# Kernel tuning notes

Hardware: AMD Instinct MI355X
Metric: run time of the kernel (lower is better)

The kernel has to match this reference:

```python
import jax, jax.numpy as jnp
import numpy as np

B, N, D, H, K = 16, 256, 64, 64, 2  # batch, nodes, d_in, d_hidden, top_k


def setup_inputs() -> dict:
    key = jax.random.key(0)
    k0, k1, k2 = jax.random.split(key, 3)
    O = jax.random.normal(k0, (B, N, D), dtype=jnp.float32)
    # PairwiseFeaturizer.proj: Linear(4*D, H) -> ReLU -> Linear(H, 1)
    W1 = jax.random.normal(k1, (4 * D, H), dtype=jnp.float32) / np.sqrt(4 * D).astype(np.float32)
    b1 = jnp.zeros((H,), dtype=jnp.float32)
    W2 = jax.random.normal(k2, (H, 1), dtype=jnp.float32) / np.sqrt(H).astype(np.float32)
    b2 = jnp.zeros((1,), dtype=jnp.float32)
    return {"O": O, "W1": W1, "b1": b1, "W2": W2, "b2": b2}


def reference(O, W1, b1, W2, b2):
    Bn, Nn, d = O.shape
    ii, jj = jnp.triu_indices(Nn, k=1)  # all undirected pairs i<j, M = N(N-1)/2
    Oi = O[:, ii, :]  # (B, M, d) gather
    Oj = O[:, jj, :]  # (B, M, d) gather
    feats = jnp.concatenate([Oi, Oj, jnp.abs(Oi - Oj), Oi * Oj], axis=-1)  # (B, M, 4d)
    h = jax.nn.relu(jnp.einsum('bmf,fh->bmh', feats, W1) + b1)
    Q = (jnp.einsum('bmh,ho->bmo', h, W2) + b2)[..., 0]  # (B, M)
    # greedy top-k selection mask (eps -> 0 limit of select_pairs)
    idx = jax.lax.top_k(Q, K)[1]  # (B, K)
    mask = jnp.zeros(Q.shape, dtype=bool).at[jnp.arange(Q.shape[0])[:, None], idx].set(True)
    return Q, mask
```

## Files before the change

kernel.cpp:

```cpp
#include <hip/hip_runtime.h>
#include <math.h>

#define Bn 16
#define Nn 256
#define Mm (Nn*(Nn-1)/2)
#define CHUNK 4080

typedef __attribute__((ext_vector_type(8))) _Float16 f16x8;
typedef __attribute__((ext_vector_type(4))) _Float16 f16x4;
typedef __attribute__((ext_vector_type(4))) float f32x4;
typedef __attribute__((ext_vector_type(16))) float f32x16;

typedef union { f16x8 v; _Float16 h[8]; unsigned u[4]; } H8;
typedef union { f16x4 v; _Float16 h[4]; } H4;

#define MFMA(acc, a, b) \
  acc = __builtin_amdgcn_mfma_f32_16x16x32_f16((a), (b), (acc), 0, 0, 0)
#define MFMA32(acc, a, b) \
  acc = __builtin_amdgcn_mfma_f32_32x32x16_f16((a), (b), (acc), 0, 0, 0)

__device__ __forceinline__ void top2_update(float v, int m,
    float& v1, int& i1, float& v2, int& i2)
{
  bool c1 = (v > v1) || (v == v1 && m < i1);
  bool c2 = (v > v2) || (v == v2 && m < i2);
  float nv2 = c1 ? v1 : (c2 ? v : v2);
  int   ni2 = c1 ? i1 : (c2 ? m : i2);
  v1 = c1 ? v : v1;  i1 = c1 ? m : i1;
  v2 = nv2;          i2 = ni2;
}

__device__ __forceinline__ int hperm(int h) {
  return (h >> 5) * 32 + ((h >> 2) & 1) * 16 + (h & 3) + 4 * ((h & 31) >> 3);
}

__global__ __launch_bounds__(256) void prep_all(
    const float* __restrict__ O, const float* __restrict__ W1,
    const float* __restrict__ b1,
    _Float16* __restrict__ wtg, _Float16* __restrict__ obg,
    float* __restrict__ Ag, _Float16* __restrict__ Cgh)
{
  const int t = threadIdx.x;
  if (blockIdx.x < 64) {
    const int h = blockIdx.x;
    wtg[h * 256 + t] = (_Float16)W1[t * 64 + h];
    return;
  }

  __shared__ __align__(16) _Float16 s_ob[64][72];
  __shared__ __align__(16) _Float16 s_w[64][136];
  const int l = t & 63, wv = t >> 6;
  const int lo = l & 15, g = l >> 4;
  const int bb = blockIdx.x - 64;
  const int b = bb >> 2, rt = bb & 3;
  const int r0 = rt * 64;
  const float* Ob = O + ((size_t)b * Nn + r0) * 64;

  #pragma unroll
  for (int p = 0; p < 4; ++p) {
    int v = t + p * 256;
    int r = v >> 4, c4 = (v & 15) * 4;
    float4 x = ((const float4*)Ob)[v];
    H4 pk; pk.h[0] = (_Float16)x.x; pk.h[1] = (_Float16)x.y;
           pk.h[2] = (_Float16)x.z; pk.h[3] = (_Float16)x.w;
    *(f16x4*)&s_ob[r][c4] = pk.v;
    *(f16x4*)&obg[((size_t)b * Nn + r0 + r) * 64 + c4] = pk.v;
  }
  #pragma unroll
  for (int p = 0; p < 32; ++p) {
    int kk = p * 4 + (t >> 6), h = t & 63;
    s_w[h][kk] = (_Float16)W1[kk * 64 + h];
  }
  __syncthreads();

  H8 aop[2];
  #pragma unroll
  for (int ks = 0; ks < 2; ++ks)
    aop[ks].v = *(const f16x8*)&s_ob[wv * 16 + lo][ks * 32 + g * 8];

  #pragma unroll
  for (int half = 0; half < 2; ++half) {
    #pragma unroll
    for (int nf = 0; nf < 4; ++nf) {
      f32x4 ac = {0.f, 0.f, 0.f, 0.f};
      #pragma unroll
      for (int ks = 0; ks < 2; ++ks) {
        H8 bop; bop.v = *(const f16x8*)&s_w[nf * 16 + lo][half * 64 + ks * 32 + g * 8];
        MFMA(ac, aop[ks].v, bop.v);
      }
      const int h  = nf * 16 + lo;
      const int px = hperm(h);
      if (half == 0) {
        float bbv = b1[h];
        #pragma unroll
        for (int r = 0; r < 4; ++r)
          Ag[((size_t)b * Nn + r0 + wv * 16 + g * 4 + r) * 64 + px] = ac[r] + bbv;
      } else {
        #pragma unroll
        for (int r = 0; r < 4; ++r)
          Cgh[((size_t)b * Nn + r0 + wv * 16 + g * 4 + r) * 64 + px] = (_Float16)ac[r];
      }
    }
  }
}

__global__ __launch_bounds__(256, 2) void pair_kernel(
    const _Float16* __restrict__ obg,
    const float* __restrict__ Ag,
    const _Float16* __restrict__ Cgh,
    const float* __restrict__ W2,
    const float* __restrict__ b2,
    const _Float16* __restrict__ wtg,
    float* __restrict__ Q,
    float* __restrict__ cand)
{
  __shared__ __align__(16) _Float16 s_wt[64][136];
  __shared__ __align__(16) _Float16 s_oi[16][72];
  __shared__ __align__(16) float s_Ap[16][68];
  __shared__ float s_w2p[64];
  __shared__ float s_red[4][4];

  const int t  = threadIdx.x;
  const int l  = t & 63, wv = t >> 6;
  const int lo32 = l & 31, hi = l >> 5;

  const int blk    = blockIdx.x;
  const int within = blk >> 3;
  const int batch  = (blk & 7) * 2 + within / 72;
  int tl           = within % 72;
  int a = 0;
  while (tl >= 8 - (a >> 1)) { tl -= 8 - (a >> 1); ++a; }
  const int c   = (a >> 1) + tl;
  const int ti0 = a * 16, tj0 = c * 32;
  const bool isdiag = (tj0 < ti0 + 16);

  const size_t obase = (size_t)batch * Nn;
  const size_t qbase = (size_t)batch * Mm;

  {
    const int h = t >> 2, kq = (t & 3) * 32;
    #pragma unroll
    for (int q = 0; q < 4; ++q)
      *(f16x8*)&s_wt[h][kq + q * 8] =
          *(const f16x8*)&wtg[h * 256 + 128 + kq + q * 8];
  }
  {
    int r = t >> 4, c4 = (t & 15) * 4;
    *(f16x4*)&s_oi[r][c4] =
        *(const f16x4*)&obg[(obase + ti0 + r) * 64 + c4];
    *(f32x4*)&s_Ap[r][c4] =
        *(const f32x4*)&Ag[(obase + ti0 + r) * 64 + c4];
    if (t < 64) s_w2p[hperm(t)] = W2[t];
  }
  __syncthreads();

  H8 wA[8], wB[8];
  #pragma unroll
  for (int s8 = 0; s8 < 8; ++s8) {
    wA[s8].v = *(const f16x8*)&s_wt[     lo32][s8 * 16 + hi * 8];
    wB[s8].v = *(const f16x8*)&s_wt[32 + lo32][s8 * 16 + hi * 8];
  }
  const int j = tj0 + lo32;
  H8 ojb[4];
  #pragma unroll
  for (int s4 = 0; s4 < 4; ++s4)
    ojb[s4].v = *(const f16x8*)&obg[(obase + j) * 64 + s4 * 16 + hi * 8];
  f32x4 cinA[4], cinB[4];
  #pragma unroll
  for (int q = 0; q < 4; ++q) {
    H4 ca; ca.v = *(const f16x4*)&Cgh[(obase + j) * 64 + hi * 16 + q * 4];
    H4 cb; cb.v = *(const f16x4*)&Cgh[(obase + j) * 64 + 32 + hi * 16 + q * 4];
    #pragma unroll
    for (int e = 0; e < 4; ++e) {
      cinA[q][e] = (float)ca.h[e];
      cinB[q][e] = (float)cb.h[e];
    }
  }

  const float b2v = b2[0];
  float v1 = -INFINITY, v2 = -INFINITY;
  int   i1 = 0x7fffffff, i2 = 0x7fffffff;

  #pragma unroll
  for (int ii = 0; ii < 4; ++ii) {
    const int iL = wv * 4 + ii;
    const int i  = ti0 + iL;

    H8 oib[4];
    #pragma unroll
    for (int s4 = 0; s4 < 4; ++s4)
      oib[s4].v = *(const f16x8*)&s_oi[iL][s4 * 16 + hi * 8];

    f32x16 accA, accB;
    #pragma unroll
    for (int q = 0; q < 4; ++q) {
      f32x4 av = *(const f32x4*)&s_Ap[iL][hi * 16 + q * 4];
      f32x4 bv = *(const f32x4*)&s_Ap[iL][32 + hi * 16 + q * 4];
      #pragma unroll
      for (int e = 0; e < 4; ++e) {
        accA[q * 4 + e] = av[e];
        accB[q * 4 + e] = bv[e];
      }
    }

    __builtin_amdgcn_s_setprio(1);
    #pragma unroll
    for (int s4 = 0; s4 < 4; ++s4) {
      H8 fd, fp;
      fd.v = oib[s4].v - ojb[s4].v;
      #pragma unroll
      for (int q = 0; q < 4; ++q) fd.u[q] &= 0x7FFF7FFFu;
      fp.v = oib[s4].v * ojb[s4].v;
      MFMA32(accA, wA[s4].v,     fd.v);
      MFMA32(accB, wB[s4].v,     fd.v);
      MFMA32(accA, wA[s4 + 4].v, fp.v);
      MFMA32(accB, wB[s4 + 4].v, fp.v);
    }
    __builtin_amdgcn_s_setprio(0);

    float pA = 0.f, pB = 0.f;
    #pragma unroll
    for (int q = 0; q < 4; ++q) {
      f32x4 wa = *(const f32x4*)&s_w2p[hi * 16 + q * 4];
      f32x4 wb = *(const f32x4*)&s_w2p[32 + hi * 16 + q * 4];
      #pragma unroll
      for (int e = 0; e < 4; ++e) {
        pA = fmaf(fmaxf(accA[q * 4 + e] + cinA[q][e], 0.f), wa[e], pA);
        pB = fmaf(fmaxf(accB[q * 4 + e] + cinB[q][e], 0.f), wb[e], pB);
      }
    }
    float part = pA + pB;
    part += __shfl_xor(part, 32);

    if (l < 32 && (!isdiag || j > i)) {
      const int mb = i * (Nn - 1) - (i * (i - 1)) / 2 - i - 1;
      const float qv = part + b2v;
      Q[qbase + mb + j] = qv;
      top2_update(qv, mb + j, v1, i1, v2, i2);
    }
  }

  #pragma unroll
  for (int s = 1; s < 64; s <<= 1) {
    float u1 = __shfl_xor(v1, s); int j1 = __shfl_xor(i1, s);
    float u2 = __shfl_xor(v2, s); int j2 = __shfl_xor(i2, s);
    top2_update(u1, j1, v1, i1, v2, i2);
    top2_update(u2, j2, v1, i1, v2, i2);
  }
  if (l == 0) {
    s_red[wv][0] = v1; s_red[wv][1] = __int_as_float(i1);
    s_red[wv][2] = v2; s_red[wv][3] = __int_as_float(i2);
  }
  __syncthreads();
  if (t == 0) {
    float a1 = s_red[0][0]; int x1 = __float_as_int(s_red[0][1]);
    float a2 = s_red[0][2]; int x2 = __float_as_int(s_red[0][3]);
    #pragma unroll
    for (int e = 1; e < 4; ++e) {
      top2_update(s_red[e][0], __float_as_int(s_red[e][1]), a1, x1, a2, x2);
      top2_update(s_red[e][2], __float_as_int(s_red[e][3]), a1, x1, a2, x2);
    }
    float* cp = cand + ((size_t)batch * 72 + within % 72) * 4;
    cp[0] = a1; cp[1] = __int_as_float(x1);
    cp[2] = a2; cp[3] = __int_as_float(x2);
  }
}

__global__ __launch_bounds__(256) void rankmask_kernel(
    const float* __restrict__ O, const float* __restrict__ W1,
    const float* __restrict__ b1, const float* __restrict__ W2,
    const float* __restrict__ cand, float* __restrict__ mask)
{
  const int b   = blockIdx.x >> 3;
  const int cch = blockIdx.x & 7;
  const int t   = threadIdx.x;
  const int wv  = t >> 6, h = t & 63;
  __shared__ float s_cv[144];
  __shared__ int   s_ci[144];
  __shared__ int   s_m[8];
  __shared__ int   s_ij[8][2];
  __shared__ float s_or[8][2][64];
  __shared__ float s_qe[8];
  __shared__ int   s_k0, s_k1;

  if (t < 144) {
    const float* cp = cand + (size_t)(b * 72 + (t >> 1)) * 4;
    s_cv[t] = cp[(t & 1) * 2];
    s_ci[t] = __float_as_int(cp[(t & 1) * 2 + 1]);
  }
  __syncthreads();
  if (t < 144) {
    float v = s_cv[t]; int m = s_ci[t];
    int rank = 0;
    for (int e = 0; e < 144; ++e) {
      float u = s_cv[e]; int n = s_ci[e];
      rank += (u > v || (u == v && n < m)) ? 1 : 0;
    }
    if (rank < 8) s_m[rank] = m;
  }
  __syncthreads();
  if (t < 16) {
    int m = s_m[t >> 1];
    int i = 0, rem = m;
    while (rem >= Nn - 1 - i) { rem -= Nn - 1 - i; ++i; }
    int j = i + 1 + rem;
    s_ij[t >> 1][t & 1] = (t & 1) ? j : i;
  }
  __syncthreads();
  {
    int cc = t >> 5, rr = (t >> 4) & 1, c4 = (t & 15) * 4;
    int row = s_ij[cc][rr];
    *(float4*)&s_or[cc][rr][c4] = *(const float4*)&O[((size_t)b * Nn + row) * 64 + c4];
  }
  __syncthreads();
  #pragma unroll
  for (int p = 0; p < 2; ++p) {
    const int cc = p * 4 + wv;
    float z = b1[h];
    #pragma unroll 8
    for (int d = 0; d < 64; ++d) {
      float oi = s_or[cc][0][d], oj = s_or[cc][1][d];
      float f3 = fabsf(oi - oj), f4 = oi * oj;
      z += oi * W1[d * 64 + h] + oj * W1[(64 + d) * 64 + h]
         + f3 * W1[(128 + d) * 64 + h] + f4 * W1[(192 + d) * 64 + h];
    }
    float part = fmaxf(z, 0.f) * W2[h];
    #pragma unroll
    for (int s = 1; s < 64; s <<= 1) part += __shfl_xor(part, s);
    if (h == 0) s_qe[cc] = part;
  }
  __syncthreads();
  if (t == 0) {
    float v1 = -INFINITY, v2 = -INFINITY;
    int   i1 = 0x7fffffff, i2 = 0x7fffffff;
    for (int e = 0; e < 8; ++e)
      top2_update(s_qe[e], s_m[e], v1, i1, v2, i2);
    s_k0 = i1; s_k1 = i2;
  }
  __syncthreads();

  const int k0 = s_k0, k1 = s_k1;
  float* mb = mask + (size_t)b * Mm;
  const int m0 = cch * CHUNK;
  for (int m = m0 + t; m < m0 + CHUNK; m += 256)
    mb[m] = (m == k0 || m == k1) ? 1.0f : 0.0f;
}

extern "C" void kernel_launch(void* const* d_in, const int* in_sizes, int n_in,
                              void* d_out, int out_size, void* d_ws, size_t ws_size,
                              hipStream_t stream) {
  const float* O  = (const float*)d_in[0];
  const float* W1 = (const float*)d_in[1];
  const float* b1 = (const float*)d_in[2];
  const float* W2 = (const float*)d_in[3];
  const float* b2 = (const float*)d_in[4];

  float* Q    = (float*)d_out;
  float* mask = Q + (size_t)Bn * Mm;

  char* ws = (char*)d_ws;
  _Float16* wtg = (_Float16*)ws;
  _Float16* obg = (_Float16*)(ws + 32768);
  float*    Ag  = (float*)(ws + 32768 + 524288);
  _Float16* Cgh = (_Float16*)(ws + 32768 + 524288 + 1048576);
  float*    cand = (float*)(ws + 32768 + 524288 + 1048576 + 524288);

  prep_all<<<dim3(128), dim3(256), 0, stream>>>(O, W1, b1, wtg, obg, Ag, Cgh);
  pair_kernel<<<dim3(Bn * 72), dim3(256), 0, stream>>>(obg, Ag, Cgh, W2, b2, wtg, Q, cand);
  rankmask_kernel<<<dim3(Bn * 8), dim3(256), 0, stream>>>(O, W1, b1, W2, cand, mask);
}
```

Measured before the change: 53.21 us.

## Stream pair-kernel operands from LDS per step to cut registers, raise occupancy

Changes the pair kernel to stop holding all W1 fragments, Oj vectors and converted C inputs in registers. The weights and O tiles now go into chunk-major LDS layouts, and each MFMA step loads its operands from LDS inside non-unrolled loops. Launch bounds move from 2 to 4 blocks per SM to raise occupancy. The cost is extra LDS traffic and loop overhead in the inner loop, and the prep kernel's weight layout changes to match.

Measured after the change: 57.80 us. 8.6% more time.

```diff
diff --git a/kernel.cpp b/kernel.cpp
--- a/kernel.cpp
+++ b/kernel.cpp
@@ -37,13 +37,16 @@
 __global__ __launch_bounds__(256) void prep_all(
     const float* __restrict__ O, const float* __restrict__ W1,
     const float* __restrict__ b1,
-    _Float16* __restrict__ wtg, _Float16* __restrict__ obg,
+    _Float16* __restrict__ wtgf, _Float16* __restrict__ obg,
     float* __restrict__ Ag, _Float16* __restrict__ Cgh)
 {
   const int t = threadIdx.x;
   if (blockIdx.x < 64) {
     const int h = blockIdx.x;
-    wtg[h * 256 + t] = (_Float16)W1[t * 64 + h];
+    if (t < 128) {
+      int c8 = t >> 3, e = t & 7;
+      wtgf[((size_t)c8 * 64 + h) * 8 + e] = (_Float16)W1[(128 + t) * 64 + h];
+    }
     return;
   }
 
@@ -104,18 +107,19 @@
   }
 }
 
-__global__ __launch_bounds__(256, 2) void pair_kernel(
+__global__ __launch_bounds__(256, 4) void pair_kernel(
     const _Float16* __restrict__ obg,
     const float* __restrict__ Ag,
     const _Float16* __restrict__ Cgh,
     const float* __restrict__ W2,
     const float* __restrict__ b2,
-    const _Float16* __restrict__ wtg,
+    const _Float16* __restrict__ wtgf,
     float* __restrict__ Q,
     float* __restrict__ cand)
 {
-  __shared__ __align__(16) _Float16 s_wt[64][136];
-  __shared__ __align__(16) _Float16 s_oi[16][72];
+  __shared__ __align__(16) _Float16 s_wf[16][64][8];
+  __shared__ __align__(16) _Float16 s_oif[8][16][8];
+  __shared__ __align__(16) _Float16 s_ojf[8][32][8];
   __shared__ __align__(16) float s_Ap[16][68];
   __shared__ float s_w2p[64];
   __shared__ float s_red[4][4];
@@ -137,59 +141,46 @@
   const size_t obase = (size_t)batch * Nn;
   const size_t qbase = (size_t)batch * Mm;
 
+  #pragma unroll
+  for (int p = 0; p < 4; ++p) {
+    int idx = t + p * 256;
+    *(f16x8*)&s_wf[0][0][idx * 8] = *(const f16x8*)&wtgf[(size_t)idx * 8];
+  }
+  if (t < 128) {
+    int c8 = t & 7, i = t >> 3;
+    *(f16x8*)&s_oif[c8][i][0] =
+        *(const f16x8*)&obg[(obase + ti0 + i) * 64 + c8 * 8];
+  }
   {
-    const int h = t >> 2, kq = (t & 3) * 32;
-    #pragma unroll
-    for (int q = 0; q < 4; ++q)
-      *(f16x8*)&s_wt[h][kq + q * 8] =
-          *(const f16x8*)&wtg[h * 256 + 128 + kq + q * 8];
+    int c8 = t & 7, j = t >> 3;
+    *(f16x8*)&s_ojf[c8][j][0] =
+        *(const f16x8*)&obg[(obase + tj0 + j) * 64 + c8 * 8];
   }
   {
     int r = t >> 4, c4 = (t & 15) * 4;
-    *(f16x4*)&s_oi[r][c4] =
-        *(const f16x4*)&obg[(obase + ti0 + r) * 64 + c4];
     *(f32x4*)&s_Ap[r][c4] =
         *(const f32x4*)&Ag[(obase + ti0 + r) * 64 + c4];
+    if (t < 64) s_w2p[t] = W2[0];
     if (t < 64) s_w2p[hperm(t)] = W2[t];
   }
   __syncthreads();
 
-  H8 wA[8], wB[8];
-  #pragma unroll
-  for (int s8 = 0; s8 < 8; ++s8) {
-    wA[s8].v = *(const f16x8*)&s_wt[     lo32][s8 * 16 + hi * 8];
-    wB[s8].v = *(const f16x8*)&s_wt[32 + lo32][s8 * 16 + hi * 8];
-  }
   const int j = tj0 + lo32;
-  H8 ojb[4];
-  #pragma unroll
-  for (int s4 = 0; s4 < 4; ++s4)
-    ojb[s4].v = *(const f16x8*)&obg[(obase + j) * 64 + s4 * 16 + hi * 8];
-  f32x4 cinA[4], cinB[4];
+  H4 cinA4[4], cinB4[4];
   #pragma unroll
   for (int q = 0; q < 4; ++q) {
-    H4 ca; ca.v = *(const f16x4*)&Cgh[(obase + j) * 64 + hi * 16 + q * 4];
-    H4 cb; cb.v = *(const f16x4*)&Cgh[(obase + j) * 64 + 32 + hi * 16 + q * 4];
-    #pragma unroll
-    for (int e = 0; e < 4; ++e) {
-      cinA[q][e] = (float)ca.h[e];
-      cinB[q][e] = (float)cb.h[e];
-    }
+    cinA4[q].v = *(const f16x4*)&Cgh[(obase + j) * 64 + hi * 16 + q * 4];
+    cinB4[q].v = *(const f16x4*)&Cgh[(obase + j) * 64 + 32 + hi * 16 + q * 4];
   }
 
   const float b2v = b2[0];
   float v1 = -INFINITY, v2 = -INFINITY;
   int   i1 = 0x7fffffff, i2 = 0x7fffffff;
 
-  #pragma unroll
+  #pragma unroll 1
   for (int ii = 0; ii < 4; ++ii) {
     const int iL = wv * 4 + ii;
     const int i  = ti0 + iL;
-
-    H8 oib[4];
-    #pragma unroll
-    for (int s4 = 0; s4 < 4; ++s4)
-      oib[s4].v = *(const f16x8*)&s_oi[iL][s4 * 16 + hi * 8];
 
     f32x16 accA, accB;
     #pragma unroll
@@ -204,17 +195,25 @@
     }
 
     __builtin_amdgcn_s_setprio(1);
-    #pragma unroll
+    #pragma unroll 1
     for (int s4 = 0; s4 < 4; ++s4) {
+      const int cw = s4 * 2 + hi;
+      H8 oi, oj, wad, wbd, wap, wbp;
+      oi.v  = *(const f16x8*)&s_oif[cw & 7][iL][0];
+      oj.v  = *(const f16x8*)&s_ojf[cw & 7][lo32][0];
+      wad.v = *(const f16x8*)&s_wf[cw][lo32][0];
+      wbd.v = *(const f16x8*)&s_wf[cw][32 + lo32][0];
+      wap.v = *(const f16x8*)&s_wf[cw + 8][lo32][0];
+      wbp.v = *(const f16x8*)&s_wf[cw + 8][32 + lo32][0];
       H8 fd, fp;
-      fd.v = oib[s4].v - ojb[s4].v;
+      fd.v = oi.v - oj.v;
       #pragma unroll
       for (int q = 0; q < 4; ++q) fd.u[q] &= 0x7FFF7FFFu;
-      fp.v = oib[s4].v * ojb[s4].v;
-      MFMA32(accA, wA[s4].v,     fd.v);
-      MFMA32(accB, wB[s4].v,     fd.v);
-      MFMA32(accA, wA[s4 + 4].v, fp.v);
-      MFMA32(accB, wB[s4 + 4].v, fp.v);
+      fp.v = oi.v * oj.v;
+      MFMA32(accA, wad.v, fd.v);
+      MFMA32(accB, wbd.v, fd.v);
+      MFMA32(accA, wap.v, fp.v);
+      MFMA32(accB, wbp.v, fp.v);
     }
     __builtin_amdgcn_s_setprio(0);
 
@@ -225,8 +224,8 @@
       f32x4 wb = *(const f32x4*)&s_w2p[32 + hi * 16 + q * 4];
       #pragma unroll
       for (int e = 0; e < 4; ++e) {
-        pA = fmaf(fmaxf(accA[q * 4 + e] + cinA[q][e], 0.f), wa[e], pA);
-        pB = fmaf(fmaxf(accB[q * 4 + e] + cinB[q][e], 0.f), wb[e], pB);
+        pA = fmaf(fmaxf(accA[q * 4 + e] + (float)cinA4[q].h[e], 0.f), wa[e], pA);
+        pB = fmaf(fmaxf(accB[q * 4 + e] + (float)cinB4[q].h[e], 0.f), wb[e], pB);
       }
     }
     float part = pA + pB;
@@ -359,13 +358,13 @@
   float* mask = Q + (size_t)Bn * Mm;
 
   char* ws = (char*)d_ws;
-  _Float16* wtg = (_Float16*)ws;
-  _Float16* obg = (_Float16*)(ws + 32768);
-  float*    Ag  = (float*)(ws + 32768 + 524288);
-  _Float16* Cgh = (_Float16*)(ws + 32768 + 524288 + 1048576);
+  _Float16* wtgf = (_Float16*)ws;
+  _Float16* obg  = (_Float16*)(ws + 32768);
+  float*    Ag   = (float*)(ws + 32768 + 524288);
+  _Float16* Cgh  = (_Float16*)(ws + 32768 + 524288 + 1048576);
   float*    cand = (float*)(ws + 32768 + 524288 + 1048576 + 524288);
 
-  prep_all<<<dim3(128), dim3(256), 0, stream>>>(O, W1, b1, wtg, obg, Ag, Cgh);
-  pair_kernel<<<dim3(Bn * 72), dim3(256), 0, stream>>>(obg, Ag, Cgh, W2, b2, wtg, Q, cand);
+  prep_all<<<dim3(128), dim3(256), 0, stream>>>(O, W1, b1, wtgf, obg, Ag, Cgh);
+  pair_kernel<<<dim3(Bn * 72), dim3(256), 0, stream>>>(obg, Ag, Cgh, W2, b2, wtgf, Q, cand);
   rankmask_kernel<<<dim3(Bn * 8), dim3(256), 0, stream>>>(O, W1, b1, W2, cand, mask);
 }
```
